# Kernel optimization log

Measured on AMD Instinct MI355X. Metric: run time of the kernel, lower is better.

The kernel has to match this reference:

```python
import jax, jax.numpy as jnp
import numpy as np

ALPHA = 0.7
BETA = 0.3
GAMMA = 4.0
SMALL_LESION_WEIGHT = 10.0
SMOOTH = 1e-05
AREA_THRESH = 100  # region.area < 100 -> small lesion


def _label_components(mask):
    """8-connectivity connected-component labeling via min-label flooding.
    mask: [B,H,W] bool. Returns int32 labels in [0, H*W) for foreground,
    H*W (sentinel) for background. Equivalent partitioning to skimage.measure.label."""
    B, H, W = mask.shape
    BIG = H * W
    ids = jnp.arange(BIG, dtype=jnp.int32).reshape(1, H, W)
    lab0 = jnp.where(mask, ids, BIG)

    def neighbor_min(lab):
        p = jnp.pad(lab, ((0, 0), (1, 1), (1, 1)), constant_values=BIG)
        m = lab
        for di in range(3):  # 3x3 window = self + 8-neighbors
            for dj in range(3):
                m = jnp.minimum(m, p[:, di:di + H, dj:dj + W])
        return jnp.where(mask, m, BIG)

    def cond(state):
        return state[1]

    def body(state):
        lab, _ = state
        new = neighbor_min(lab)
        return new, jnp.any(new != lab)

    lab, _ = jax.lax.while_loop(cond, body, (lab0, jnp.array(True)))
    return lab


def _small_lesion_weights(targets):
    """targets: [B,1,H,W] float. Returns [B,1,H,W] weights: small_lesion_weight on
    pixels of connected components with area < AREA_THRESH, else 1.0."""
    t = targets[:, 0]                      # [B,H,W]
    mask = t > 0.5
    B, H, W = mask.shape
    BIG = H * W
    lab = _label_components(mask)          # [B,H,W] int32
    flat_lab = lab.reshape(B, BIG)
    ones = mask.astype(jnp.float32).reshape(B, BIG)
    # per-image component areas; background pixels fall into segment BIG
    areas = jax.vmap(lambda l, o: jax.ops.segment_sum(o, l, num_segments=BIG + 1))(flat_lab, ones)
    pix_area = jnp.take_along_axis(areas, flat_lab, axis=1).reshape(B, H, W)
    small = mask & (pix_area < AREA_THRESH)
    w = jnp.where(small, SMALL_LESION_WEIGHT, 1.0)
    return w[:, None, :, :]


def _bce_with_logits(x, t):
    # numerically stable elementwise BCE-with-logits
    return jnp.maximum(x, 0.0) - x * t + jnp.log1p(jnp.exp(-jnp.abs(x)))


def setup_inputs() -> dict:
    key = jax.random.key(0)
    k1, k2 = jax.random.split(key)
    B, C, H, W = 8, 1, 1024, 1024
    predictions = jax.random.normal(k1, (B, C, H, W), dtype=jnp.float32)
    targets = (jax.random.uniform(k2, (B, C, H, W)) < 0.05).astype(jnp.float32)
    return {"predictions": predictions, "targets": targets}


def reference(predictions, targets):
    p = jax.nn.sigmoid(predictions)

    # dice loss (global)
    inter = jnp.sum(p * targets)
    union = jnp.sum(p) + jnp.sum(targets)
    dice_loss = 1.0 - (2.0 * inter + SMOOTH) / (union + SMOOTH)

    # focal loss from logits
    bce = _bce_with_logits(predictions, targets)
    is_pos = targets == 1
    p_t = jnp.where(is_pos, p, 1.0 - p)
    alpha_t = jnp.where(is_pos, ALPHA, 1.0 - ALPHA)
    focal_loss = jnp.mean(alpha_t * (1.0 - p_t) ** GAMMA * bce)

    # tversky loss (FN-focused)
    TP = inter
    FP = jnp.sum((1.0 - targets) * p)
    FN = jnp.sum(targets * (1.0 - p))
    tversky_loss = 1.0 - (TP + SMOOTH) / (TP + ALPHA * FP + BETA * FN + SMOOTH)

    # small-lesion weighted BCE (weights are a non-diff function of targets)
    w = _small_lesion_weights(jax.lax.stop_gradient(targets))
    small_lesion_loss = jnp.mean(w * bce)

    return (dice_loss + focal_loss + tversky_loss + small_lesion_loss) / 4.0
```

## Files before the change

kernel.cpp:

```cpp
#include <hip/hip_runtime.h>

static constexpr int Bb = 8, Hh = 1024, Ww = 1024;
static constexpr int HW     = Hh * Ww;
static constexpr int NPIX   = Bb * HW;
static constexpr int NWORDS = NPIX / 64;
static constexpr int WPR    = Ww / 64;
static constexpr int WPI    = HW / 64;
static constexpr int NBK = 2048, NT = 256;
static constexpr int FNT = 1024;
static constexpr int FBG = 256;
static constexpr int CAP = 4096;

typedef unsigned int u32;
typedef unsigned long long u64;

__device__ inline u32 lab_load(u32* L, u32 i) {
    return __hip_atomic_load(&L[i], __ATOMIC_RELAXED, __HIP_MEMORY_SCOPE_AGENT);
}
__device__ inline void lab_store(u32* L, u32 i, u32 v) {
    __hip_atomic_store(&L[i], v, __ATOMIC_RELAXED, __HIP_MEMORY_SCOPE_AGENT);
}
__device__ inline u32 find_root(u32* L, u32 x) {
    while (true) {
        u32 p = lab_load(L, x);
        if (p >= (u32)NPIX || p == x) return x;
        x = p;
    }
}
__device__ inline void union_labels(u32* L, u32 a, u32 b) {
    while (true) {
        a = find_root(L, a);
        b = find_root(L, b);
        if (a == b) return;
        if (a < b) { u32 t = a; a = b; b = t; }
        u32 old = atomicMin(&L[a], b);
        if (old == a || old >= (u32)NPIX) return;
        a = old;
    }
}

static constexpr u32 POISON = 0xAAAAAAAAu;
static constexpr u32 FLAGVAL = 0xC0FFEE00u;

__device__ inline double block_reduce(double v, double* lds) {
    for (int o = 32; o > 0; o >>= 1) v += __shfl_down(v, o, 64);
    int wave = threadIdx.x >> 6, lane = threadIdx.x & 63;
    __syncthreads();
    if (lane == 0) lds[wave] = v;
    __syncthreads();
    double r = 0.0;
    if (threadIdx.x == 0)
        for (int w = 0; w < (int)(blockDim.x >> 6); ++w) r += lds[w];
    return r;
}

__device__ inline float bce_pos(float x) {
    return fmaxf(-x, 0.0f) + __logf(1.0f + __expf(-fabsf(x)));
}

__device__ inline u64 spread4(u64 x) {
    x &= 0xFFFFull;
    x = (x | (x << 24)) & 0x000000FF000000FFull;
    x = (x | (x << 12)) & 0x000F000F000F000Full;
    x = (x | (x << 6))  & 0x0303030303030303ull;
    x = (x | (x << 3))  & 0x1111111111111111ull;
    return x;
}

__device__ inline void grid_barrier(u32* ctr, u32* flag) {
    __syncthreads();
    if (threadIdx.x == 0) {
        u32 old = __hip_atomic_fetch_add(ctr, 1u, __ATOMIC_RELAXED,
                                         __HIP_MEMORY_SCOPE_AGENT);
        if (old == POISON + (u32)FBG - 1u) {
            __hip_atomic_store(flag, FLAGVAL, __ATOMIC_RELAXED,
                               __HIP_MEMORY_SCOPE_AGENT);
        } else {
            while (__hip_atomic_load(flag, __ATOMIC_RELAXED,
                                     __HIP_MEMORY_SCOPE_AGENT) == POISON)
                __builtin_amdgcn_s_sleep(8);
        }
    }
    __syncthreads();
}

__global__ __launch_bounds__(NT) void k_init(const float4* __restrict__ pred4,
                                             const float4* __restrict__ targ4,
                                             u64* __restrict__ mask,
                                             double* __restrict__ part) {
    __shared__ double lds[NT / 64];
    float s_p = 0.f, s_t = 0.f, s_pt = 0.f, s_f = 0.f, s_b = 0.f, s_bf = 0.f;
    const int lane = threadIdx.x & 63;
    const int wid  = (blockIdx.x * NT + threadIdx.x) >> 6;

    float4 pv[4], tv[4];
    #pragma unroll
    for (int c = 0; c < 4; ++c) {
        const int chunk = (wid << 2) + c;
        pv[c] = pred4[chunk * 64 + lane];
        tv[c] = targ4[chunk * 64 + lane];
    }
    #pragma unroll
    for (int c = 0; c < 4; ++c) {
        const int chunk = (wid << 2) + c;
        const float* xa = &pv[c].x;
        const float* ta = &tv[c].x;
        u32 nib = 0;
        #pragma unroll
        for (int b = 0; b < 4; ++b) {
            const float x = xa[b], t = ta[b];
            const float ee  = __expf(-fabsf(x));
            const float rin = __builtin_amdgcn_rcpf(1.0f + ee);
            const float p   = (x >= 0.0f) ? rin : 1.0f - rin;
            const float bce = fmaxf(x, 0.0f) - x * t + __logf(1.0f + ee);
            const bool  pos = t > 0.5f;
            const float q1  = pos ? (1.0f - p) : p;
            const float at  = pos ? 0.7f : 0.3f;
            const float q2  = q1 * q1;
            s_p  += p;
            s_t  += t;
            s_pt += pos ? p : 0.0f;
            s_f  += at * q2 * q2 * bce;
            s_b  += bce;
            s_bf += pos ? bce : 0.0f;
            if (pos) nib |= 1u << b;
        }
        const u64 B0 = __ballot(nib & 1u);
        const u64 B1 = __ballot(nib & 2u);
        const u64 B2 = __ballot(nib & 4u);
        const u64 B3 = __ballot(nib & 8u);
        const int k = lane & 3;
        const u64 W = spread4(B0 >> (16 * k)) | (spread4(B1 >> (16 * k)) << 1)
                    | (spread4(B2 >> (16 * k)) << 2) | (spread4(B3 >> (16 * k)) << 3);
        if (lane < 4) mask[(chunk << 2) + lane] = W;
    }
    double r;
    r = block_reduce((double)s_p,  lds); if (threadIdx.x == 0) part[0 * NBK + blockIdx.x] = r;
    r = block_reduce((double)s_t,  lds); if (threadIdx.x == 0) part[1 * NBK + blockIdx.x] = r;
    r = block_reduce((double)s_pt, lds); if (threadIdx.x == 0) part[2 * NBK + blockIdx.x] = r;
    r = block_reduce((double)s_f,  lds); if (threadIdx.x == 0) part[3 * NBK + blockIdx.x] = r;
    r = block_reduce((double)s_b,  lds); if (threadIdx.x == 0) part[4 * NBK + blockIdx.x] = r;
    r = block_reduce((double)s_bf, lds); if (threadIdx.x == 0) part[5 * NBK + blockIdx.x] = r;
}

struct Nbr { u64 L, R, U, UL, UR, D, DL, DR; };
__device__ inline Nbr neighbors(const u64* __restrict__ mask, int wi, u64 cur) {
    int y  = (wi & (WPI - 1)) >> 4;
    int wx = wi & (WPR - 1);
    u64 lf = wx > 0       ? mask[wi - 1] : 0;
    u64 rt = wx < WPR - 1 ? mask[wi + 1] : 0;
    u64 up = 0, ul = 0, ur = 0, dn = 0, dl = 0, dr = 0;
    if (y > 0) {
        up = mask[wi - WPR];
        ul = wx > 0       ? mask[wi - WPR - 1] : 0;
        ur = wx < WPR - 1 ? mask[wi - WPR + 1] : 0;
    }
    if (y < Hh - 1) {
        dn = mask[wi + WPR];
        dl = wx > 0       ? mask[wi + WPR - 1] : 0;
        dr = wx < WPR - 1 ? mask[wi + WPR + 1] : 0;
    }
    Nbr n;
    n.L  = (cur << 1) | (lf >> 63);
    n.R  = (cur >> 1) | (rt << 63);
    n.U  = up;
    n.UL = (up << 1) | (ul >> 63);
    n.UR = (up >> 1) | (ur << 63);
    n.D  = dn;
    n.DL = (dn << 1) | (dl >> 63);
    n.DR = (dn >> 1) | (dr << 63);
    return n;
}

__device__ inline u64 half_mask(int t) {
    return (t & 1) ? 0xFFFFFFFF00000000ull : 0x00000000FFFFFFFFull;
}

static constexpr int B_CTR1 = 0, B_FLAG1 = 32, B_CTR2 = 64, B_FLAG2 = 96, B_DONE = 128;

__global__ __launch_bounds__(FNT, 4) void k_fused(const u64* __restrict__ mask,
                                                  u32* __restrict__ lab,
                                                  u32* __restrict__ area,
                                                  const float* __restrict__ pred,
                                                  double* __restrict__ part,
                                                  u32* __restrict__ bar,
                                                  float* __restrict__ out) {
    __shared__ double lds[FNT / 64];
    __shared__ int lastFlag;
    __shared__ u32 wl[CAP];
    __shared__ u32 wl_n;
    double* part_large = part + 6 * NBK;

    const int t  = blockIdx.x * FNT + threadIdx.x;
    const int wi = t >> 1;
    const u64 hm = half_mask(t);
    const u64 cur = mask[wi];
    const int base = wi << 6;

    if (threadIdx.x == 0) wl_n = 0;

    u64 nonIso = 0;
    u64 nL = 0, nU = 0, nUL = 0, nUR = 0;
    if (cur & hm) {
        Nbr n = neighbors(mask, wi, cur);
        nonIso = cur & (n.L | n.R | n.U | n.UL | n.UR | n.D | n.DL | n.DR) & hm;
        nL = n.L; nU = n.U; nUL = n.UL; nUR = n.UR;
    }
    __syncthreads();

    u64 ovf = 0;
    {
        int cnt = __builtin_popcountll(nonIso);
        if (cnt) {
            u32 slot = atomicAdd(&wl_n, (u32)cnt);
            u64 w = nonIso;
            while (w) {
                int b = __builtin_ctzll(w); w &= w - 1;
                if (slot < (u32)CAP) {
                    const u32 f = (u32)((nL >> b) & 1) | ((u32)((nU >> b) & 1) << 1)
                                | ((u32)((nUL >> b) & 1) << 2)
                                | ((u32)((nUR >> b) & 1) << 3);
                    wl[slot] = ((u32)(base + b) << 4) | f;
                } else {
                    ovf |= 1ull << b;
                }
                ++slot;
            }
        }
    }
    __syncthreads();
    const u32 nwl = wl_n < (u32)CAP ? wl_n : (u32)CAP;

    for (u32 e = threadIdx.x; e < nwl; e += FNT) {
        const u32 ent = wl[e];
        const u32 i = ent >> 4, f = ent & 15u;
        if (f & 1u) union_labels(lab, i, i - 1);
        if (f & 2u) union_labels(lab, i, i - Ww);
        else {
            if (f & 4u) union_labels(lab, i, i - Ww - 1);
            if (f & 8u) union_labels(lab, i, i - Ww + 1);
        }
    }
    {
        u64 w = ovf;
        while (w) {
            int b = __builtin_ctzll(w); w &= w - 1;
            const u64 bit = 1ull << b;
            const u32 i = base + b;
            if (nL & bit) union_labels(lab, i, i - 1);
            if (nU & bit) union_labels(lab, i, i - Ww);
            else {
                if (nUL & bit) union_labels(lab, i, i - Ww - 1);
                if (nUR & bit) union_labels(lab, i, i - Ww + 1);
            }
        }
    }
    grid_barrier(bar + B_CTR1, bar + B_FLAG1);

    for (u32 e = threadIdx.x; e < nwl; e += FNT) {
        const u32 i = wl[e] >> 4;
        const u32 r = find_root(lab, i);
        lab_store(lab, i, r);
        atomicAdd(&area[r], 1u);
    }
    {
        u64 w = ovf;
        while (w) {
            int b = __builtin_ctzll(w); w &= w - 1;
            const u32 i = base + b;
            const u32 r = find_root(lab, i);
            lab_store(lab, i, r);
            atomicAdd(&area[r], 1u);
        }
    }
    grid_barrier(bar + B_CTR2, bar + B_FLAG2);

    float s = 0.f;
    for (u32 e = threadIdx.x; e < nwl; e += FNT) {
        const u32 i = wl[e] >> 4;
        const u32 r = lab_load(lab, i);
        const u32 cnt = __hip_atomic_load(&area[r], __ATOMIC_RELAXED,
                                          __HIP_MEMORY_SCOPE_AGENT) - POISON;
        if (cnt >= 100u)
            s += bce_pos(pred[i]);
    }
    {
        u64 w = ovf;
        while (w) {
            int b = __builtin_ctzll(w); w &= w - 1;
            const u32 i = base + b;
            const u32 r = lab_load(lab, i);
            const u32 cnt = __hip_atomic_load(&area[r], __ATOMIC_RELAXED,
                                              __HIP_MEMORY_SCOPE_AGENT) - POISON;
            if (cnt >= 100u) s += bce_pos(pred[i]);
        }
    }
    double rr = block_reduce((double)s, lds);
    if (threadIdx.x == 0) {
        __hip_atomic_store(&part_large[blockIdx.x], rr, __ATOMIC_RELAXED,
                           __HIP_MEMORY_SCOPE_AGENT);
        asm volatile("s_waitcnt vmcnt(0)" ::: "memory");
        u32 old = __hip_atomic_fetch_add(bar + B_DONE, 1u, __ATOMIC_RELAXED,
                                         __HIP_MEMORY_SCOPE_AGENT);
        lastFlag = (old == POISON + (u32)FBG - 1u);
    }
    __syncthreads();
    if (!lastFlag) return;

    double sv[7] = {0, 0, 0, 0, 0, 0, 0};
    for (int j = threadIdx.x; j < NBK; j += FNT)
        #pragma unroll
        for (int k = 0; k < 6; ++k) sv[k] += part[k * NBK + j];
    for (int j = threadIdx.x; j < FBG; j += FNT)
        sv[6] += __hip_atomic_load(&part_large[j], __ATOMIC_RELAXED,
                                   __HIP_MEMORY_SCOPE_AGENT);
    double red[7];
    #pragma unroll
    for (int k = 0; k < 7; ++k) red[k] = block_reduce(sv[k], lds);
    if (threadIdx.x == 0) {
        double sum_p = red[0], sum_t = red[1], inter = red[2];
        double sum_f = red[3], sum_b = red[4], sum_bf = red[5], large_b = red[6];
        double small_b = sum_bf - large_b;
        double N = (double)NPIX;
        double dice    = 1.0 - (2.0 * inter + 1e-5) / (sum_p + sum_t + 1e-5);
        double focal   = sum_f / N;
        double FP = sum_p - inter, FN = sum_t - inter;
        double tversky = 1.0 - (inter + 1e-5) / (inter + 0.7 * FP + 0.3 * FN + 1e-5);
        double small   = (sum_b + 9.0 * small_b) / N;
        out[0] = (float)((dice + focal + tversky + small) * 0.25);
    }
}

extern "C" void kernel_launch(void* const* d_in, const int* in_sizes, int n_in,
                              void* d_out, int out_size, void* d_ws, size_t ws_size,
                              hipStream_t stream) {
    const float* pred = (const float*)d_in[0];
    const float* targ = (const float*)d_in[1];
    float* out = (float*)d_out;

    char* ws = (char*)d_ws;
    double* part = (double*)ws;
    u64* mask = (u64*)(ws + (size_t)(6 * NBK + FBG) * sizeof(double));
    u32* lab  = (u32*)(mask + NWORDS);
    u32* area = lab + NPIX;
    u32* bar  = area + NPIX;

    k_init <<<NBK, NT, 0, stream>>>((const float4*)pred, (const float4*)targ, mask, part);
    k_fused<<<FBG, FNT, 0, stream>>>(mask, lab, area, pred, part, bar, out);
}
```

Measured before the change: 140.4 us.

## Do block-local union-find in LDS and merge only boundary components globally

Each block now owns a strip of 16 image rows and runs union-find on a shared-memory label array. Component areas are accumulated locally. Only components that touch the strip's top or bottom edge are unioned into the global label array and counted in global area atomics. Purely local components are classified as large or small entirely in LDS. This is meant to cut global atomics and pointer chasing through global memory, at the cost of 64KB of dynamic LDS per block, a changed grid shape (512x512), and a global fallback path when the worklist overflows.

```diff
diff --git a/kernel.cpp b/kernel.cpp
--- a/kernel.cpp
+++ b/kernel.cpp
@@ -1,4 +1,7 @@
 #include <hip/hip_runtime.h>
+
+typedef unsigned int u32;
+typedef unsigned long long u64;
 
 static constexpr int Bb = 8, Hh = 1024, Ww = 1024;
 static constexpr int HW     = Hh * Ww;
@@ -7,12 +10,16 @@
 static constexpr int WPR    = Ww / 64;
 static constexpr int WPI    = HW / 64;
 static constexpr int NBK = 2048, NT = 256;
-static constexpr int FNT = 1024;
-static constexpr int FBG = 256;
-static constexpr int CAP = 4096;
-
-typedef unsigned int u32;
-typedef unsigned long long u64;
+static constexpr int FNT = 512, FBG = 512;
+static constexpr int SWORDS = NWORDS / FBG;
+static constexpr int SPX    = SWORDS * 64;
+static constexpr int CAP    = 2048;
+
+static constexpr u32 POISON  = 0xAAAAAAAAu;
+static constexpr u32 FLAGVAL = 0xC0FFEE00u;
+static constexpr u32 LBITS  = 0x3FFFu;
+static constexpr u32 BIGF   = 1u << 29;
+static constexpr u32 CROSSF = 1u << 30;
 
 __device__ inline u32 lab_load(u32* L, u32 i) {
     return __hip_atomic_load(&L[i], __ATOMIC_RELAXED, __HIP_MEMORY_SCOPE_AGENT);
@@ -39,8 +46,26 @@
     }
 }
 
-static constexpr u32 POISON = 0xAAAAAAAAu;
-static constexpr u32 FLAGVAL = 0xC0FFEE00u;
+__device__ inline u32 lds_load(u32* L, u32 x) {
+    return __hip_atomic_load(&L[x], __ATOMIC_RELAXED, __HIP_MEMORY_SCOPE_WORKGROUP);
+}
+__device__ inline void lds_store(u32* L, u32 x, u32 v) {
+    __hip_atomic_store(&L[x], v, __ATOMIC_RELAXED, __HIP_MEMORY_SCOPE_WORKGROUP);
+}
+__device__ inline u32 lfind2(u32* L, u32 x) {
+    while (true) { u32 p = lds_load(L, x) & LBITS; if (p == x) return x; x = p; }
+}
+__device__ inline void lunion(u32* L, u32 a, u32 b) {
+    while (true) {
+        a = lfind2(L, a);
+        b = lfind2(L, b);
+        if (a == b) return;
+        if (a < b) { u32 t = a; a = b; b = t; }
+        u32 old = atomicMin(&L[a], b);
+        if (old == a) return;
+        a = old;
+    }
+}
 
 __device__ inline double block_reduce(double v, double* lds) {
     for (int o = 32; o > 0; o >>= 1) v += __shfl_down(v, o, 64);
@@ -185,30 +210,30 @@
                                                   double* __restrict__ part,
                                                   u32* __restrict__ bar,
                                                   float* __restrict__ out) {
-    __shared__ double lds[FNT / 64];
-    __shared__ int lastFlag;
+    extern __shared__ u32 llab[];
     __shared__ u32 wl[CAP];
     __shared__ u32 wl_n;
     double* part_large = part + 6 * NBK;
 
-    const int t  = blockIdx.x * FNT + threadIdx.x;
-    const int wi = t >> 1;
-    const u64 hm = half_mask(t);
-    const u64 cur = mask[wi];
-    const int base = wi << 6;
-
-    if (threadIdx.x == 0) wl_n = 0;
-
-    u64 nonIso = 0;
-    u64 nL = 0, nU = 0, nUL = 0, nUR = 0;
+    const int tid   = threadIdx.x;
+    const int lwi   = tid >> 1;
+    const int wi    = blockIdx.x * SWORDS + lwi;
+    const int spx   = blockIdx.x * SPX;
+    const u64 hm    = half_mask(tid);
+    const u64 cur   = mask[wi];
+    const int lbase = lwi << 6;
+
+    if (tid == 0) wl_n = 0;
+
+    u64 nonIso = 0, nL = 0, nU = 0, nUL = 0, nUR = 0, nDany = 0;
     if (cur & hm) {
         Nbr n = neighbors(mask, wi, cur);
         nonIso = cur & (n.L | n.R | n.U | n.UL | n.UR | n.D | n.DL | n.DR) & hm;
         nL = n.L; nU = n.U; nUL = n.UL; nUR = n.UR;
-    }
-    __syncthreads();
-
-    u64 ovf = 0;
+        nDany = n.D | n.DL | n.DR;
+    }
+    __syncthreads();
+
     {
         int cnt = __builtin_popcountll(nonIso);
         if (cnt) {
@@ -216,108 +241,156 @@
             u64 w = nonIso;
             while (w) {
                 int b = __builtin_ctzll(w); w &= w - 1;
+                const u32 li = (u32)(lbase + b);
+                llab[li] = li;
                 if (slot < (u32)CAP) {
-                    const u32 f = (u32)((nL >> b) & 1) | ((u32)((nU >> b) & 1) << 1)
+                    const u32 f = (u32)((nL  >> b) & 1)
+                                | ((u32)((nU  >> b) & 1) << 1)
                                 | ((u32)((nUL >> b) & 1) << 2)
-                                | ((u32)((nUR >> b) & 1) << 3);
-                    wl[slot] = ((u32)(base + b) << 4) | f;
-                } else {
-                    ovf |= 1ull << b;
+                                | ((u32)((nUR >> b) & 1) << 3)
+                                | ((u32)((nDany >> b) & 1) << 4);
+                    wl[slot] = (li << 5) | f;
                 }
                 ++slot;
             }
         }
     }
     __syncthreads();
-    const u32 nwl = wl_n < (u32)CAP ? wl_n : (u32)CAP;
-
-    for (u32 e = threadIdx.x; e < nwl; e += FNT) {
-        const u32 ent = wl[e];
-        const u32 i = ent >> 4, f = ent & 15u;
-        if (f & 1u) union_labels(lab, i, i - 1);
-        if (f & 2u) union_labels(lab, i, i - Ww);
-        else {
-            if (f & 4u) union_labels(lab, i, i - Ww - 1);
-            if (f & 8u) union_labels(lab, i, i - Ww + 1);
-        }
-    }
-    {
-        u64 w = ovf;
+    const bool fb  = wl_n > (u32)CAP;
+    const u32 nwl  = fb ? 0u : wl_n;
+
+    if (!fb) {
+        for (u32 e = tid; e < nwl; e += FNT) {
+            const u32 ent = wl[e], li = ent >> 5, f = ent & 31u;
+            const u32 ris = li >> 10;
+            if (f & 1u) lunion(llab, li, li - 1);
+            if (ris > 0) {
+                if (f & 2u) lunion(llab, li, li - 1024);
+                else {
+                    if (f & 4u) lunion(llab, li, li - 1025);
+                    if (f & 8u) lunion(llab, li, li - 1023);
+                }
+            }
+        }
+        __syncthreads();
+        for (u32 e = tid; e < nwl; e += FNT) {
+            const u32 ent = wl[e], li = ent >> 5, f = ent & 31u;
+            const u32 ris = li >> 10;
+            const u32 r = lfind2(llab, li);
+            if (r != li) lds_store(llab, li, r);
+            atomicAdd(&llab[r], 1u << 14);
+            const u32 gi = (u32)spx + li;
+            if (ris == 0 && (f & (2u | 4u | 8u))) {
+                atomicOr(&llab[r], CROSSF);
+                const u32 gr = (u32)spx + r;
+                if (f & 2u) union_labels(lab, gr, gi - Ww);
+                if (f & 4u) union_labels(lab, gr, gi - Ww - 1);
+                if (f & 8u) union_labels(lab, gr, gi - Ww + 1);
+            }
+            if (ris == 15 && (f & 16u)) {
+                atomicOr(&llab[r], CROSSF);
+                union_labels(lab, gi, (u32)spx + r);
+            }
+        }
+    } else {
+        u64 w = cur & (nL | nU | nUL | nUR) & hm;
         while (w) {
             int b = __builtin_ctzll(w); w &= w - 1;
             const u64 bit = 1ull << b;
-            const u32 i = base + b;
-            if (nL & bit) union_labels(lab, i, i - 1);
-            if (nU & bit) union_labels(lab, i, i - Ww);
+            const u32 gi = (u32)(spx + lbase + b);
+            if (nL & bit) union_labels(lab, gi, gi - 1);
+            if (nU & bit) union_labels(lab, gi, gi - Ww);
             else {
-                if (nUL & bit) union_labels(lab, i, i - Ww - 1);
-                if (nUR & bit) union_labels(lab, i, i - Ww + 1);
+                if (nUL & bit) union_labels(lab, gi, gi - Ww - 1);
+                if (nUR & bit) union_labels(lab, gi, gi - Ww + 1);
             }
         }
     }
     grid_barrier(bar + B_CTR1, bar + B_FLAG1);
 
-    for (u32 e = threadIdx.x; e < nwl; e += FNT) {
-        const u32 i = wl[e] >> 4;
-        const u32 r = find_root(lab, i);
-        lab_store(lab, i, r);
-        atomicAdd(&area[r], 1u);
-    }
-    {
-        u64 w = ovf;
+    if (!fb) {
+        for (u32 e = tid; e < nwl; e += FNT) {
+            const u32 li = wl[e] >> 5;
+            const u32 ent = lds_load(llab, li);
+            if ((ent & LBITS) != li) continue;
+            if (ent & CROSSF) {
+                const u32 gr = find_root(lab, (u32)spx + li);
+                lab_store(lab, (u32)spx + li, gr);
+                atomicAdd(&area[gr], (ent >> 14) & 0x7FFFu);
+            } else if (((ent >> 14) & 0x7FFFu) >= 100u) {
+                atomicOr(&llab[li], BIGF);
+            }
+        }
+    } else {
+        u64 w = nonIso;
         while (w) {
             int b = __builtin_ctzll(w); w &= w - 1;
-            const u32 i = base + b;
-            const u32 r = find_root(lab, i);
-            lab_store(lab, i, r);
+            const u32 gi = (u32)(spx + lbase + b);
+            const u32 r = find_root(lab, gi);
+            lab_store(lab, gi, r);
             atomicAdd(&area[r], 1u);
         }
     }
     grid_barrier(bar + B_CTR2, bar + B_FLAG2);
 
     float s = 0.f;
-    for (u32 e = threadIdx.x; e < nwl; e += FNT) {
-        const u32 i = wl[e] >> 4;
-        const u32 r = lab_load(lab, i);
-        const u32 cnt = __hip_atomic_load(&area[r], __ATOMIC_RELAXED,
-                                          __HIP_MEMORY_SCOPE_AGENT) - POISON;
-        if (cnt >= 100u)
-            s += bce_pos(pred[i]);
-    }
-    {
-        u64 w = ovf;
+    if (!fb) {
+        for (u32 e = tid; e < nwl; e += FNT) {
+            const u32 li = wl[e] >> 5;
+            const u32 ent = lds_load(llab, li);
+            if ((ent & LBITS) == li && (ent & CROSSF)) {
+                const u32 gr  = lab_load(lab, (u32)spx + li);
+                const u32 tot = __hip_atomic_load(&area[gr], __ATOMIC_RELAXED,
+                                                  __HIP_MEMORY_SCOPE_AGENT) - POISON;
+                if (tot >= 100u) atomicOr(&llab[li], BIGF);
+            }
+        }
+        __syncthreads();
+        for (u32 e = tid; e < nwl; e += FNT) {
+            const u32 li = wl[e] >> 5;
+            const u32 ent = lds_load(llab, li);
+            const u32 r = ent & LBITS;
+            const u32 fl = (r == li) ? ent : lds_load(llab, r);
+            if (fl & BIGF) s += bce_pos(pred[spx + li]);
+        }
+    } else {
+        u64 w = nonIso;
         while (w) {
             int b = __builtin_ctzll(w); w &= w - 1;
-            const u32 i = base + b;
-            const u32 r = lab_load(lab, i);
+            const u32 gi = (u32)(spx + lbase + b);
+            const u32 r = lab_load(lab, gi);
             const u32 cnt = __hip_atomic_load(&area[r], __ATOMIC_RELAXED,
                                               __HIP_MEMORY_SCOPE_AGENT) - POISON;
-            if (cnt >= 100u) s += bce_pos(pred[i]);
-        }
-    }
-    double rr = block_reduce((double)s, lds);
-    if (threadIdx.x == 0) {
+            if (cnt >= 100u) s += bce_pos(pred[gi]);
+        }
+    }
+    __syncthreads();
+    double* rlds   = (double*)llab;
+    int* lastFlagP = (int*)&llab[32];
+
+    double rr = block_reduce((double)s, rlds);
+    if (tid == 0) {
         __hip_atomic_store(&part_large[blockIdx.x], rr, __ATOMIC_RELAXED,
                            __HIP_MEMORY_SCOPE_AGENT);
         asm volatile("s_waitcnt vmcnt(0)" ::: "memory");
         u32 old = __hip_atomic_fetch_add(bar + B_DONE, 1u, __ATOMIC_RELAXED,
                                          __HIP_MEMORY_SCOPE_AGENT);
-        lastFlag = (old == POISON + (u32)FBG - 1u);
-    }
-    __syncthreads();
-    if (!lastFlag) return;
+        *lastFlagP = (old == POISON + (u32)FBG - 1u);
+    }
+    __syncthreads();
+    if (!*lastFlagP) return;
 
     double sv[7] = {0, 0, 0, 0, 0, 0, 0};
-    for (int j = threadIdx.x; j < NBK; j += FNT)
+    for (int j = tid; j < NBK; j += FNT)
         #pragma unroll
         for (int k = 0; k < 6; ++k) sv[k] += part[k * NBK + j];
-    for (int j = threadIdx.x; j < FBG; j += FNT)
+    for (int j = tid; j < FBG; j += FNT)
         sv[6] += __hip_atomic_load(&part_large[j], __ATOMIC_RELAXED,
                                    __HIP_MEMORY_SCOPE_AGENT);
     double red[7];
     #pragma unroll
-    for (int k = 0; k < 7; ++k) red[k] = block_reduce(sv[k], lds);
-    if (threadIdx.x == 0) {
+    for (int k = 0; k < 7; ++k) red[k] = block_reduce(sv[k], rlds);
+    if (tid == 0) {
         double sum_p = red[0], sum_t = red[1], inter = red[2];
         double sum_f = red[3], sum_b = red[4], sum_bf = red[5], large_b = red[6];
         double small_b = sum_bf - large_b;
@@ -346,5 +419,6 @@
     u32* bar  = area + NPIX;
 
     k_init <<<NBK, NT, 0, stream>>>((const float4*)pred, (const float4*)targ, mask, part);
-    k_fused<<<FBG, FNT, 0, stream>>>(mask, lab, area, pred, part, bar, out);
-}
+    k_fused<<<FBG, FNT, (size_t)SPX * sizeof(u32), stream>>>(mask, lab, area, pred,
+                                                             part, bar, out);
+}
```

Result: faster. 136.4 us (-2.8%).
